# Kernel tuning notes

Measured on AMD Instinct MI355X. Metric: run time of the kernel, lower is better.

## Reference

```python
import jax, jax.numpy as jnp
import numpy as np

B, L, D_MODEL, H, DK, DV = 4, 2048, 1024, 16, 64, 64


def setup_inputs() -> dict:
    key = jax.random.key(0)
    ks = jax.random.split(key, 11)
    s = 1.0 / np.sqrt(D_MODEL)
    return {
        "queries": jax.random.normal(ks[0], (B, L, D_MODEL), jnp.float32),
        "keys": jax.random.normal(ks[1], (B, L, D_MODEL), jnp.float32),
        "values": jax.random.normal(ks[2], (B, L, D_MODEL), jnp.float32),
        "Wq": jax.random.normal(ks[3], (D_MODEL, H * DK), jnp.float32) * s,
        "bq": jnp.zeros((H * DK,), jnp.float32),
        "Wk": jax.random.normal(ks[4], (D_MODEL, H * DK), jnp.float32) * s,
        "bk": jnp.zeros((H * DK,), jnp.float32),
        "Wv": jax.random.normal(ks[5], (D_MODEL, H * DV), jnp.float32) * s,
        "bv": jnp.zeros((H * DV,), jnp.float32),
        "Wo": jax.random.normal(ks[6], (H * DV, D_MODEL), jnp.float32) * s,
        "bo": jnp.zeros((D_MODEL,), jnp.float32),
    }


def reference(queries, keys, values, Wq, bq, Wk, bk, Wv, bv, Wo, bo):
    b, l, _ = queries.shape
    s = keys.shape[1]
    q = (queries @ Wq + bq).reshape(b, l, H, DK)
    k = (keys @ Wk + bk).reshape(b, s, H, DK)
    v = (values @ Wv + bv).reshape(b, s, H, DV)
    scale = 1.0 / np.sqrt(DK)
    scores = jnp.einsum("blhe,bshe->bhls", q, k)  # [B,H,L,S]
    causal = jnp.triu(jnp.ones((l, s), bool), k=1)
    scores = jnp.where(causal[None, None], -jnp.inf, scores)
    A = jax.nn.softmax(scale * scores, axis=-1)
    out = jnp.einsum("bhls,bshd->blhd", A, v).reshape(b, l, H * DV)
    return out @ Wo + bo
```

## Files before the change

kernel.cpp:

```cpp
#include <hip/hip_runtime.h>

typedef __attribute__((ext_vector_type(8))) short s8v;
typedef __attribute__((ext_vector_type(4))) short s4v;
typedef __attribute__((ext_vector_type(4))) float f4v;
typedef __attribute__((ext_vector_type(4))) unsigned int u4v;

#define LOG2E 1.44269504088896340736f

__device__ __forceinline__ unsigned short f2bf(float f) {
    unsigned int x = __float_as_uint(f);
    return (unsigned short)((x + 0x7fffu + ((x >> 16) & 1u)) >> 16);
}
__device__ __forceinline__ s8v ld8(const unsigned short* p) {
    return *(const s8v*)p;
}

#define GLOAD_LDS(g, l) __builtin_amdgcn_global_load_lds(              \
    (const __attribute__((address_space(1))) void*)(const void*)(g),   \
    (__attribute__((address_space(3))) void*)(void*)(l), 16, 0, 0)

__global__ __launch_bounds__(256) void transpose_w4(
    const float* __restrict__ W0, const float* __restrict__ W1,
    const float* __restrict__ W2, const float* __restrict__ W3,
    unsigned short* __restrict__ T0, unsigned short* __restrict__ T1,
    unsigned short* __restrict__ T2, unsigned short* __restrict__ T3)
{
    __shared__ float tile[32][33];
    int z = blockIdx.z;
    const float* W = z == 0 ? W0 : z == 1 ? W1 : z == 2 ? W2 : W3;
    unsigned short* Wt = z == 0 ? T0 : z == 1 ? T1 : z == 2 ? T2 : T3;
    int tx = threadIdx.x, ty = threadIdx.y;
    int x = blockIdx.x * 32 + tx;
#pragma unroll
    for (int i = 0; i < 4; i++) {
        int y = blockIdx.y * 32 + ty + i * 8;
        tile[ty + i * 8][tx] = W[y * 1024 + x];
    }
    __syncthreads();
    int x2 = blockIdx.y * 32 + tx;
#pragma unroll
    for (int i = 0; i < 4; i++) {
        int y2 = blockIdx.x * 32 + ty + i * 8;
        Wt[y2 * 1024 + x2] = f2bf(tile[tx][ty + i * 8]);
    }
}

__global__ __launch_bounds__(256) void qkv_gemm(
    const float* __restrict__ Aq, const float* __restrict__ Ak,
    const float* __restrict__ Avv,
    const unsigned short* __restrict__ BtQ, const unsigned short* __restrict__ BtK,
    const unsigned short* __restrict__ BtV,
    const float* __restrict__ bq, const float* __restrict__ bk,
    const float* __restrict__ bv,
    unsigned short* __restrict__ qo, unsigned short* __restrict__ ko,
    unsigned short* __restrict__ vo, float sscale)
{
    __shared__ __align__(16) unsigned short ldsA[2][128 * 32];
    __shared__ __align__(16) unsigned short ldsB[2][128 * 32];

    int i = blockIdx.x;
    int c = i & 7, j = i >> 3;
    int bx = j & 7, zy = c * 24 + (j >> 3);
    int z = zy >> 6, by = zy & 63;

    const float* A = z == 0 ? Aq : z == 1 ? Ak : Avv;
    const unsigned short* Bt = z == 0 ? BtQ : z == 1 ? BtK : BtV;
    const float* bias = z == 0 ? bq : z == 1 ? bk : bv;
    unsigned short* out = z == 0 ? qo : z == 1 ? ko : vo;
    float oscale = z == 0 ? sscale : 1.0f;

    int tid = threadIdx.x;
    int w = tid >> 6, lane = tid & 63;
    int quad = lane >> 4, l15 = lane & 15;
    int wr = w >> 1, wc = w & 1;
    int m0 = by * 128, n0 = bx * 128;

    int arow = tid >> 1, ahs = tid & 1;
    int crow = tid >> 2, ck = (tid & 3) * 8;

    const float* ap = A + (size_t)(m0 + arow) * 1024 + ahs * 16;
    const unsigned short* bp = Bt + (size_t)(n0 + crow) * 1024 + ck;
    unsigned short* aw0 = &ldsA[0][arow * 32 + ahs * 16];
    unsigned short* aw1 = &ldsA[1][arow * 32 + ahs * 16];

    f4v acc[4][4];
#pragma unroll
    for (int m = 0; m < 4; m++)
#pragma unroll
        for (int n = 0; n < 4; n++) { f4v zz = {0.f, 0.f, 0.f, 0.f}; acc[m][n] = zz; }

    auto stageB = [&](int buf, int k0) {
        GLOAD_LDS(bp + k0, &ldsB[buf][w * 512]);
        GLOAD_LDS(bp + k0 + (size_t)64 * 1024, &ldsB[buf][2048 + w * 512]);
    };
    auto cvtwrA = [&](unsigned short* dst, f4v a0, f4v a1, f4v a2, f4v a3) {
        unsigned int w0, w1, w2, w3, w4, w5, w6, w7;
        asm("v_cvt_pk_bf16_f32 %0, %1, %2" : "=v"(w0) : "v"(a0[0]), "v"(a0[1]));
        asm("v_cvt_pk_bf16_f32 %0, %1, %2" : "=v"(w1) : "v"(a0[2]), "v"(a0[3]));
        asm("v_cvt_pk_bf16_f32 %0, %1, %2" : "=v"(w2) : "v"(a1[0]), "v"(a1[1]));
        asm("v_cvt_pk_bf16_f32 %0, %1, %2" : "=v"(w3) : "v"(a1[2]), "v"(a1[3]));
        asm("v_cvt_pk_bf16_f32 %0, %1, %2" : "=v"(w4) : "v"(a2[0]), "v"(a2[1]));
        asm("v_cvt_pk_bf16_f32 %0, %1, %2" : "=v"(w5) : "v"(a2[2]), "v"(a2[3]));
        asm("v_cvt_pk_bf16_f32 %0, %1, %2" : "=v"(w6) : "v"(a3[0]), "v"(a3[1]));
        asm("v_cvt_pk_bf16_f32 %0, %1, %2" : "=v"(w7) : "v"(a3[2]), "v"(a3[3]));
        u4v lo; lo[0] = w0; lo[1] = w1; lo[2] = w2; lo[3] = w3;
        u4v hi; hi[0] = w4; hi[1] = w5; hi[2] = w6; hi[3] = w7;
        *(u4v*)dst = lo;
        *(u4v*)(dst + 8) = hi;
    };

    {
        f4v a0 = *(const f4v*)(ap), a1 = *(const f4v*)(ap + 4);
        f4v a2 = *(const f4v*)(ap + 8), a3 = *(const f4v*)(ap + 12);
        stageB(0, 0);
        cvtwrA(aw0, a0, a1, a2, a3);
    }
    __syncthreads();

    for (int t = 0; t < 32; t++) {
        int buf = t & 1;
        bool pf = t < 31;
        f4v a0, a1, a2, a3;
        if (pf) {
            const float* an = ap + (t + 1) * 32;
            a0 = *(const f4v*)(an); a1 = *(const f4v*)(an + 4);
            a2 = *(const f4v*)(an + 8); a3 = *(const f4v*)(an + 12);
            stageB(buf ^ 1, (t + 1) * 32);
        }
        s8v af[4], bfr[4];
#pragma unroll
        for (int m = 0; m < 4; m++)
            af[m] = *(const s8v*)&ldsA[buf][(wr * 64 + m * 16 + l15) * 32 + quad * 8];
#pragma unroll
        for (int n = 0; n < 4; n++)
            bfr[n] = *(const s8v*)&ldsB[buf][(wc * 64 + n * 16 + l15) * 32 + quad * 8];
#pragma unroll
        for (int m = 0; m < 4; m++)
#pragma unroll
            for (int n = 0; n < 4; n++)
                acc[m][n] = __builtin_amdgcn_mfma_f32_16x16x32_bf16(af[m], bfr[n], acc[m][n], 0, 0, 0);
        if (pf) cvtwrA(buf ? aw0 : aw1, a0, a1, a2, a3);
        __syncthreads();
    }

#pragma unroll
    for (int n = 0; n < 4; n++) {
        int col = n0 + wc * 64 + n * 16 + l15;
        float bvf = bias[col];
#pragma unroll
        for (int m = 0; m < 4; m++) {
#pragma unroll
            for (int r = 0; r < 4; r++) {
                int row = m0 + wr * 64 + m * 16 + quad * 4 + r;
                float v = (acc[m][n][r] + bvf) * oscale;
                int bb = row >> 11, l = row & 2047;
                int hh = col >> 6, d = col & 63;
                if (z != 2) {
                    out[(((size_t)bb * 16 + hh) * 2048 + l) * 64 + d] = f2bf(v);
                } else {
                    int jj = l & 63;
                    int s = ((jj & 0x0C) << 2) | ((jj & 0x02) << 2) |
                            ((jj & 0x30) >> 3) | (jj & 1);
                    int lp = (l & ~63) | s;
                    out[(((size_t)bb * 16 + hh) * 64 + d) * 2048 + lp] = f2bf(v);
                }
            }
        }
    }
}

__global__ __launch_bounds__(256) void ogemm(
    const unsigned short* __restrict__ A,
    const unsigned short* __restrict__ Bt,
    const float* __restrict__ bias,
    float* __restrict__ out)
{
    __shared__ __align__(16) unsigned short ldsA[2][128 * 32];
    __shared__ __align__(16) unsigned short ldsB[2][128 * 32];

    int i = blockIdx.x;
    int c = i & 7, j = i >> 3;
    int bx = j & 7, by = c * 8 + (j >> 3);

    int tid = threadIdx.x;
    int w = tid >> 6, lane = tid & 63;
    int quad = lane >> 4, l15 = lane & 15;
    int wr = w >> 1, wc = w & 1;
    int m0 = by * 128, n0 = bx * 128;

    int crow = tid >> 2, ck = (tid & 3) * 8;

    f4v acc[4][4];
#pragma unroll
    for (int m = 0; m < 4; m++)
#pragma unroll
        for (int n = 0; n < 4; n++) { f4v zz = {0.f, 0.f, 0.f, 0.f}; acc[m][n] = zz; }

    auto stage = [&](int buf, int k0) {
        const unsigned short* ga = A + (size_t)(m0 + crow) * 1024 + k0 + ck;
        GLOAD_LDS(ga, &ldsA[buf][w * 512]);
        GLOAD_LDS(ga + (size_t)64 * 1024, &ldsA[buf][2048 + w * 512]);
        const unsigned short* gb = Bt + (size_t)(n0 + crow) * 1024 + k0 + ck;
        GLOAD_LDS(gb, &ldsB[buf][w * 512]);
        GLOAD_LDS(gb + (size_t)64 * 1024, &ldsB[buf][2048 + w * 512]);
    };

    stage(0, 0);
    __syncthreads();
    for (int t = 0; t < 32; t++) {
        int buf = t & 1;
        if (t < 31) stage(buf ^ 1, (t + 1) * 32);
        s8v af[4], bfr[4];
#pragma unroll
        for (int m = 0; m < 4; m++)
            af[m] = *(const s8v*)&ldsA[buf][(wr * 64 + m * 16 + l15) * 32 + quad * 8];
#pragma unroll
        for (int n = 0; n < 4; n++)
            bfr[n] = *(const s8v*)&ldsB[buf][(wc * 64 + n * 16 + l15) * 32 + quad * 8];
#pragma unroll
        for (int m = 0; m < 4; m++)
#pragma unroll
            for (int n = 0; n < 4; n++)
                acc[m][n] = __builtin_amdgcn_mfma_f32_16x16x32_bf16(af[m], bfr[n], acc[m][n], 0, 0, 0);
        __syncthreads();
    }

#pragma unroll
    for (int n = 0; n < 4; n++) {
        int col = n0 + wc * 64 + n * 16 + l15;
        float bvf = bias[col];
#pragma unroll
        for (int m = 0; m < 4; m++)
#pragma unroll
            for (int r = 0; r < 4; r++) {
                int row = m0 + wr * 64 + m * 16 + quad * 4 + r;
                out[(size_t)row * 1024 + col] = acc[m][n][r] + bvf;
            }
    }
}

__global__ __launch_bounds__(256) void attn_kernel(
    const unsigned short* __restrict__ Q,
    const unsigned short* __restrict__ K,
    const unsigned short* __restrict__ Vt,
    unsigned short* __restrict__ O)
{
    __shared__ __align__(16) unsigned short Kb[2][64 * 64];
    __shared__ __align__(16) unsigned short Vb[2][64 * 64];

    int tid = threadIdx.x;
    int w = tid >> 6, lane = tid & 63;
    int quad = lane >> 4, l15 = lane & 15;

    int bid = blockIdx.x;
    int swz = (bid & 7) * 128 + (bid >> 3);
    int xp = swz & 15;
    int h = (swz >> 4) & 15;
    int b = swz >> 8;
    int bh = b * 16 + h;

    int srow = tid >> 3;
    int soff = ((tid & 7) * 16) ^ ((srow & 7) << 4);
    const unsigned short* Kbase = K + (size_t)bh * 2048 * 64;
    const unsigned short* Vbase = Vt + (size_t)bh * 64 * 2048;

    auto stageK = [&](int buf, int kt) {
        const unsigned short* g1 = Kbase + (size_t)(kt * 64 + srow) * 64 + (soff >> 1);
        GLOAD_LDS(g1, &Kb[buf][w * 512]);
        GLOAD_LDS(g1 + (size_t)32 * 64, &Kb[buf][2048 + w * 512]);
    };
    auto stageV = [&](int buf, int kt) {
        const unsigned short* g1 = Vbase + (size_t)srow * 2048 + kt * 64 + (soff >> 1);
        GLOAD_LDS(g1, &Vb[buf][w * 512]);
        GLOAD_LDS(g1 + (size_t)32 * 2048, &Vb[buf][2048 + w * 512]);
    };

    int rswz = (l15 & 7) << 4;

#pragma unroll 1
    for (int half = 0; half < 2; half++) {
        int qt = half ? 31 - xp : xp;
        int m0 = qt * 64 + w * 16;

        const unsigned short* qb = Q + ((size_t)bh * 2048 + m0 + l15) * 64 + quad * 8;
        s8v aq0 = ld8(qb), aq1 = ld8(qb + 32);

        float mrun = -1e30f, lsum = 0.f;
        f4v oacc[4];
#pragma unroll
        for (int t = 0; t < 4; t++) { f4v z = {0.f, 0.f, 0.f, 0.f}; oacc[t] = z; }

        stageK(0, 0);
        stageV(0, 0);
        __syncthreads();

#pragma unroll 1
        for (int kt = 0; kt <= qt; kt++) {
            int buf = kt & 1;
            if (kt < qt) { stageK(buf ^ 1, kt + 1); stageV(buf ^ 1, kt + 1); }

            f4v sacc[4];
#pragma unroll
            for (int t = 0; t < 4; t++) { f4v z = {0.f, 0.f, 0.f, 0.f}; sacc[t] = z; }
            const char* kbp = (const char*)&Kb[buf][0];
#pragma unroll
            for (int t = 0; t < 4; t++) {
                int rb = (t * 16 + l15) * 128;
                s8v k0 = *(const s8v*)(kbp + rb + ((quad * 16) ^ rswz));
                s8v k1 = *(const s8v*)(kbp + rb + ((64 + quad * 16) ^ rswz));
                sacc[t] = __builtin_amdgcn_mfma_f32_16x16x32_bf16(k0, aq0, sacc[t], 0, 0, 0);
                sacc[t] = __builtin_amdgcn_mfma_f32_16x16x32_bf16(k1, aq1, sacc[t], 0, 0, 0);
            }

            if (kt == qt) {
                int qrow = w * 16 + l15;
#pragma unroll
                for (int t = 0; t < 4; t++)
#pragma unroll
                    for (int r = 0; r < 4; r++) {
                        int key = t * 16 + quad * 4 + r;
                        if (key > qrow) sacc[t][r] = -1e30f;
                    }
            }

            float mx = sacc[0][0];
#pragma unroll
            for (int t = 0; t < 4; t++)
#pragma unroll
                for (int r = 0; r < 4; r++)
                    mx = fmaxf(mx, sacc[t][r]);
            mx = fmaxf(mx, __shfl_xor(mx, 16));
            mx = fmaxf(mx, __shfl_xor(mx, 32));

            if (__any(mx > mrun + 8.0f)) {
                float mnew = fmaxf(mrun, mx);
                float alpha = exp2f(mrun - mnew);
                lsum *= alpha;
#pragma unroll
                for (int r = 0; r < 4; r++) {
                    float ar = __shfl(alpha, quad * 4 + r);
#pragma unroll
                    for (int t2 = 0; t2 < 4; t2++) oacc[t2][r] *= ar;
                }
                mrun = mnew;
            }

            float rs = 0.f;
#pragma unroll
            for (int t = 0; t < 4; t++)
#pragma unroll
                for (int r = 0; r < 4; r++) {
                    float p = exp2f(sacc[t][r] - mrun);
                    rs += p;
                    sacc[t][r] = p;
                }
            lsum += rs;

            unsigned int pwv[4][2];
#pragma unroll
            for (int t = 0; t < 4; t++) {
                asm("v_cvt_pk_bf16_f32 %0, %1, %2"
                    : "=v"(pwv[t][0]) : "v"(sacc[t][0]), "v"(sacc[t][1]));
                asm("v_cvt_pk_bf16_f32 %0, %1, %2"
                    : "=v"(pwv[t][1]) : "v"(sacc[t][2]), "v"(sacc[t][3]));
            }

            const char* vbp = (const char*)&Vb[buf][0];
#pragma unroll
            for (int c = 0; c < 2; c++) {
                u4v aw;
                aw[0] = pwv[0][c]; aw[1] = pwv[1][c];
                aw[2] = pwv[2][c]; aw[3] = pwv[3][c];
                s8v apf = __builtin_bit_cast(s8v, aw);
#pragma unroll
                for (int t2 = 0; t2 < 4; t2++) {
                    int rb = (t2 * 16 + l15) * 128;
                    s8v bvv = *(const s8v*)(vbp + rb + ((quad * 32 + c * 16) ^ rswz));
                    oacc[t2] = __builtin_amdgcn_mfma_f32_16x16x32_bf16(apf, bvv, oacc[t2], 0, 0, 0);
                }
            }
            __syncthreads();
        }

        float ltot = lsum;
        ltot += __shfl_xor(ltot, 16);
        ltot += __shfl_xor(ltot, 32);
        float inv = 1.f / ltot;
#pragma unroll
        for (int r = 0; r < 4; r++) {
            float ir = __shfl(inv, quad * 4 + r);
            int l = m0 + quad * 4 + r;
#pragma unroll
            for (int t2 = 0; t2 < 4; t2++) {
                O[((size_t)b * 2048 + l) * 1024 + h * 64 + t2 * 16 + l15] = f2bf(oacc[t2][r] * ir);
            }
        }
    }
}

extern "C" void kernel_launch(void* const* d_in, const int* in_sizes, int n_in,
                              void* d_out, int out_size, void* d_ws, size_t ws_size,
                              hipStream_t stream)
{
    const float* queries = (const float*)d_in[0];
    const float* keys    = (const float*)d_in[1];
    const float* values  = (const float*)d_in[2];
    const float* Wq = (const float*)d_in[3];
    const float* bq = (const float*)d_in[4];
    const float* Wk = (const float*)d_in[5];
    const float* bk = (const float*)d_in[6];
    const float* Wv = (const float*)d_in[7];
    const float* bv = (const float*)d_in[8];
    const float* Wo = (const float*)d_in[9];
    const float* bo = (const float*)d_in[10];

    unsigned short* ws = (unsigned short*)d_ws;
    const size_t M1 = 1u << 20, M8 = 8u << 20;
    unsigned short* WqT = ws;
    unsigned short* WkT = ws + 1 * M1;
    unsigned short* WvT = ws + 2 * M1;
    unsigned short* WoT = ws + 3 * M1;
    unsigned short* qw  = ws + 4 * M1;
    unsigned short* kw  = qw + M8;
    unsigned short* vtw = kw + M8;
    unsigned short* ow  = vtw + M8;

    const float sscale = 0.125f * LOG2E;

    dim3 tb(32, 8);
    transpose_w4<<<dim3(32, 32, 4), tb, 0, stream>>>(
        Wq, Wk, Wv, Wo, WqT, WkT, WvT, WoT);

    qkv_gemm<<<dim3(1536), 256, 0, stream>>>(
        queries, keys, values, WqT, WkT, WvT, bq, bk, bv,
        qw, kw, vtw, sscale);

    attn_kernel<<<dim3(1024), 256, 0, stream>>>(qw, kw, vtw, ow);

    ogemm<<<dim3(512), 256, 0, stream>>>(ow, WoT, bo, (float*)d_out);
}
```

Baseline: 391.7 us.

## Enlarge QKV GEMM tiles to 256x256 with 512 threads and swizzled A LDS

Grows the fused QKV projection GEMM block tile from 128x128 to 256x256, running 8 waves per block with a 128x64 sub-tile per wave. The grid shrinks from 1536 to 384 blocks with a new block-to-tile mapping. The larger tile is meant to cut global and LDS traffic per MFMA through more operand reuse. A new XOR swizzle on the A tile in LDS is meant to avoid bank conflicts on the fragment reads. In exchange it raises register pressure and LDS use, and 384 blocks spread unevenly over the CUs, which can leave a tail of idle units.

```diff
diff --git a/kernel.cpp b/kernel.cpp
--- a/kernel.cpp
+++ b/kernel.cpp
@@ -45,7 +45,7 @@
     }
 }
 
-__global__ __launch_bounds__(256) void qkv_gemm(
+__global__ __launch_bounds__(512) void qkv_gemm(
     const float* __restrict__ Aq, const float* __restrict__ Ak,
     const float* __restrict__ Avv,
     const unsigned short* __restrict__ BtQ, const unsigned short* __restrict__ BtK,
@@ -55,45 +55,48 @@
     unsigned short* __restrict__ qo, unsigned short* __restrict__ ko,
     unsigned short* __restrict__ vo, float sscale)
 {
-    __shared__ __align__(16) unsigned short ldsA[2][128 * 32];
-    __shared__ __align__(16) unsigned short ldsB[2][128 * 32];
+    __shared__ __align__(16) unsigned short ldsA[2][256 * 32];
+    __shared__ __align__(16) unsigned short ldsB[2][256 * 32];
 
     int i = blockIdx.x;
     int c = i & 7, j = i >> 3;
-    int bx = j & 7, zy = c * 24 + (j >> 3);
-    int z = zy >> 6, by = zy & 63;
-
+    int by = c * 4 + (j & 3);
+    int bx = j >> 2;
+
+    int z = bx >> 2;
     const float* A = z == 0 ? Aq : z == 1 ? Ak : Avv;
     const unsigned short* Bt = z == 0 ? BtQ : z == 1 ? BtK : BtV;
     const float* bias = z == 0 ? bq : z == 1 ? bk : bv;
     unsigned short* out = z == 0 ? qo : z == 1 ? ko : vo;
     float oscale = z == 0 ? sscale : 1.0f;
 
+    int m0 = by * 256;
+    int n0 = (bx & 3) * 256;
+
     int tid = threadIdx.x;
     int w = tid >> 6, lane = tid & 63;
     int quad = lane >> 4, l15 = lane & 15;
-    int wr = w >> 1, wc = w & 1;
-    int m0 = by * 128, n0 = bx * 128;
-
-    int arow = tid >> 1, ahs = tid & 1;
-    int crow = tid >> 2, ck = (tid & 3) * 8;
-
-    const float* ap = A + (size_t)(m0 + arow) * 1024 + ahs * 16;
-    const unsigned short* bp = Bt + (size_t)(n0 + crow) * 1024 + ck;
-    unsigned short* aw0 = &ldsA[0][arow * 32 + ahs * 16];
-    unsigned short* aw1 = &ldsA[1][arow * 32 + ahs * 16];
-
-    f4v acc[4][4];
-#pragma unroll
-    for (int m = 0; m < 4; m++)
+    int wr = w >> 2, wc = w & 3;
+
+    int arow = tid >> 1, ahalf = tid & 1;
+    const float* ap = A + (size_t)(m0 + arow) * 1024 + ahalf * 16;
+    int ab = arow * 64 + ahalf * 32;
+    int aswz = (arow & 7) << 4;
+    int awb0 = ab ^ aswz, awb1 = (ab + 16) ^ aswz;
+
+    const unsigned short* bp = Bt + (size_t)(n0 + (tid >> 2)) * 1024 + (tid & 3) * 8;
+
+    f4v acc[8][4];
+#pragma unroll
+    for (int m = 0; m < 8; m++)
 #pragma unroll
         for (int n = 0; n < 4; n++) { f4v zz = {0.f, 0.f, 0.f, 0.f}; acc[m][n] = zz; }
 
     auto stageB = [&](int buf, int k0) {
         GLOAD_LDS(bp + k0, &ldsB[buf][w * 512]);
-        GLOAD_LDS(bp + k0 + (size_t)64 * 1024, &ldsB[buf][2048 + w * 512]);
+        GLOAD_LDS(bp + k0 + (size_t)128 * 1024, &ldsB[buf][4096 + w * 512]);
     };
-    auto cvtwrA = [&](unsigned short* dst, f4v a0, f4v a1, f4v a2, f4v a3) {
+    auto cvtwrA = [&](int buf, f4v a0, f4v a1, f4v a2, f4v a3) {
         unsigned int w0, w1, w2, w3, w4, w5, w6, w7;
         asm("v_cvt_pk_bf16_f32 %0, %1, %2" : "=v"(w0) : "v"(a0[0]), "v"(a0[1]));
         asm("v_cvt_pk_bf16_f32 %0, %1, %2" : "=v"(w1) : "v"(a0[2]), "v"(a0[3]));
@@ -105,15 +108,18 @@
         asm("v_cvt_pk_bf16_f32 %0, %1, %2" : "=v"(w7) : "v"(a3[2]), "v"(a3[3]));
         u4v lo; lo[0] = w0; lo[1] = w1; lo[2] = w2; lo[3] = w3;
         u4v hi; hi[0] = w4; hi[1] = w5; hi[2] = w6; hi[3] = w7;
-        *(u4v*)dst = lo;
-        *(u4v*)(dst + 8) = hi;
+        char* base = (char*)&ldsA[buf][0];
+        *(u4v*)(base + awb0) = lo;
+        *(u4v*)(base + awb1) = hi;
     };
 
+    int rswzA = (l15 & 7) << 4;
+
     {
-        f4v a0 = *(const f4v*)(ap), a1 = *(const f4v*)(ap + 4);
+        f4v a0 = *(const f4v*)ap, a1 = *(const f4v*)(ap + 4);
         f4v a2 = *(const f4v*)(ap + 8), a3 = *(const f4v*)(ap + 12);
         stageB(0, 0);
-        cvtwrA(aw0, a0, a1, a2, a3);
+        cvtwrA(0, a0, a1, a2, a3);
     }
     __syncthreads();
 
@@ -123,23 +129,26 @@
         f4v a0, a1, a2, a3;
         if (pf) {
             const float* an = ap + (t + 1) * 32;
-            a0 = *(const f4v*)(an); a1 = *(const f4v*)(an + 4);
+            a0 = *(const f4v*)an; a1 = *(const f4v*)(an + 4);
             a2 = *(const f4v*)(an + 8); a3 = *(const f4v*)(an + 12);
             stageB(buf ^ 1, (t + 1) * 32);
         }
-        s8v af[4], bfr[4];
-#pragma unroll
-        for (int m = 0; m < 4; m++)
-            af[m] = *(const s8v*)&ldsA[buf][(wr * 64 + m * 16 + l15) * 32 + quad * 8];
+        const char* abase = (const char*)&ldsA[buf][0];
+        s8v af[8], bfr[4];
+#pragma unroll
+        for (int m = 0; m < 8; m++) {
+            int row = wr * 128 + m * 16 + l15;
+            af[m] = *(const s8v*)(abase + ((row * 64 + quad * 16) ^ rswzA));
+        }
 #pragma unroll
         for (int n = 0; n < 4; n++)
             bfr[n] = *(const s8v*)&ldsB[buf][(wc * 64 + n * 16 + l15) * 32 + quad * 8];
 #pragma unroll
-        for (int m = 0; m < 4; m++)
+        for (int m = 0; m < 8; m++)
 #pragma unroll
             for (int n = 0; n < 4; n++)
                 acc[m][n] = __builtin_amdgcn_mfma_f32_16x16x32_bf16(af[m], bfr[n], acc[m][n], 0, 0, 0);
-        if (pf) cvtwrA(buf ? aw0 : aw1, a0, a1, a2, a3);
+        if (pf) cvtwrA(buf ^ 1, a0, a1, a2, a3);
         __syncthreads();
     }
 
@@ -147,14 +156,14 @@
     for (int n = 0; n < 4; n++) {
         int col = n0 + wc * 64 + n * 16 + l15;
         float bvf = bias[col];
-#pragma unroll
-        for (int m = 0; m < 4; m++) {
+        int hh = col >> 6, d = col & 63;
+#pragma unroll
+        for (int m = 0; m < 8; m++) {
 #pragma unroll
             for (int r = 0; r < 4; r++) {
-                int row = m0 + wr * 64 + m * 16 + quad * 4 + r;
+                int row = m0 + wr * 128 + m * 16 + quad * 4 + r;
                 float v = (acc[m][n][r] + bvf) * oscale;
                 int bb = row >> 11, l = row & 2047;
-                int hh = col >> 6, d = col & 63;
                 if (z != 2) {
                     out[(((size_t)bb * 16 + hh) * 2048 + l) * 64 + d] = f2bf(v);
                 } else {
@@ -431,7 +440,7 @@
     transpose_w4<<<dim3(32, 32, 4), tb, 0, stream>>>(
         Wq, Wk, Wv, Wo, WqT, WkT, WvT, WoT);
 
-    qkv_gemm<<<dim3(1536), 256, 0, stream>>>(
+    qkv_gemm<<<dim3(384), 512, 0, stream>>>(
         queries, keys, values, WqT, WkT, WvT, bq, bk, bv,
         qw, kw, vtw, sscale);
 
```

Result: slower. 405.5 us (+3.5%).

## Triple-buffer GEMM LDS stages with swizzled layout and explicit waitcnt barriers

Applied to the files above, without the earlier changes.

Both the QKV projection GEMM and the output GEMM move from double to triple LDS buffering, prefetching two K-steps ahead. The single __syncthreads per step becomes explicit vmcnt/lgkmcnt waits plus s_barrier, and the MFMA block is wrapped in s_setprio. The LDS tiles get an XOR swizzle on 16-byte chunks to cut bank conflicts, and the QKV block-to-tile mapping is reordered so that z selects contiguous block ranges. The attention softmax max and sum become tree reductions to shorten dependency chains. In exchange, LDS use goes up, which may lower occupancy, and the hand-tuned wait counts are easy to get wrong.

```diff
diff --git a/kernel.cpp b/kernel.cpp
--- a/kernel.cpp
+++ b/kernel.cpp
@@ -45,7 +45,7 @@
     }
 }
 
-__global__ __launch_bounds__(256) void qkv_gemm(
+__global__ __launch_bounds__(256) void qkv_fused(
     const float* __restrict__ Aq, const float* __restrict__ Ak,
     const float* __restrict__ Avv,
     const unsigned short* __restrict__ BtQ, const unsigned short* __restrict__ BtK,
@@ -55,13 +55,14 @@
     unsigned short* __restrict__ qo, unsigned short* __restrict__ ko,
     unsigned short* __restrict__ vo, float sscale)
 {
-    __shared__ __align__(16) unsigned short ldsA[2][128 * 32];
-    __shared__ __align__(16) unsigned short ldsB[2][128 * 32];
+    __shared__ __align__(16) unsigned short ldsA[3][128 * 32];
+    __shared__ __align__(16) unsigned short ldsB[3][128 * 32];
 
     int i = blockIdx.x;
-    int c = i & 7, j = i >> 3;
-    int bx = j & 7, zy = c * 24 + (j >> 3);
-    int z = zy >> 6, by = zy & 63;
+    int z = i >> 9;
+    int r = i & 511;
+    int c = r & 7, j = r >> 3;
+    int bx = j & 7, by = c * 8 + (j >> 3);
 
     const float* A = z == 0 ? Aq : z == 1 ? Ak : Avv;
     const unsigned short* Bt = z == 0 ? BtQ : z == 1 ? BtK : BtV;
@@ -75,13 +76,15 @@
     int wr = w >> 1, wc = w & 1;
     int m0 = by * 128, n0 = bx * 128;
 
-    int arow = tid >> 1, ahs = tid & 1;
-    int crow = tid >> 2, ck = (tid & 3) * 8;
-
-    const float* ap = A + (size_t)(m0 + arow) * 1024 + ahs * 16;
-    const unsigned short* bp = Bt + (size_t)(n0 + crow) * 1024 + ck;
-    unsigned short* aw0 = &ldsA[0][arow * 32 + ahs * 16];
-    unsigned short* aw1 = &ldsA[1][arow * 32 + ahs * 16];
+    int r1 = tid >> 2, qp = tid & 3;
+    int qs = (qp ^ (r1 & 3)) * 8;
+    const unsigned short* gb1 = Bt + (size_t)(n0 + r1) * 1024 + qs;
+    const unsigned short* gb2 = Bt + (size_t)(n0 + r1 + 64) * 1024 + qs;
+
+    int arow = tid >> 1, ahalf = tid & 1;
+    const float* ap = A + (size_t)(m0 + arow) * 1024 + ahalf * 16;
+    int awb0 = arow * 64 + (((2 * ahalf)     ^ (arow & 3)) << 4);
+    int awb1 = arow * 64 + (((2 * ahalf + 1) ^ (arow & 3)) << 4);
 
     f4v acc[4][4];
 #pragma unroll
@@ -90,10 +93,10 @@
         for (int n = 0; n < 4; n++) { f4v zz = {0.f, 0.f, 0.f, 0.f}; acc[m][n] = zz; }
 
     auto stageB = [&](int buf, int k0) {
-        GLOAD_LDS(bp + k0, &ldsB[buf][w * 512]);
-        GLOAD_LDS(bp + k0 + (size_t)64 * 1024, &ldsB[buf][2048 + w * 512]);
+        GLOAD_LDS(gb1 + k0, &ldsB[buf][w * 512]);
+        GLOAD_LDS(gb2 + k0, &ldsB[buf][2048 + w * 512]);
     };
-    auto cvtwrA = [&](unsigned short* dst, f4v a0, f4v a1, f4v a2, f4v a3) {
+    auto cvtwrA = [&](int buf, f4v a0, f4v a1, f4v a2, f4v a3) {
         unsigned int w0, w1, w2, w3, w4, w5, w6, w7;
         asm("v_cvt_pk_bf16_f32 %0, %1, %2" : "=v"(w0) : "v"(a0[0]), "v"(a0[1]));
         asm("v_cvt_pk_bf16_f32 %0, %1, %2" : "=v"(w1) : "v"(a0[2]), "v"(a0[3]));
@@ -105,78 +108,98 @@
         asm("v_cvt_pk_bf16_f32 %0, %1, %2" : "=v"(w7) : "v"(a3[2]), "v"(a3[3]));
         u4v lo; lo[0] = w0; lo[1] = w1; lo[2] = w2; lo[3] = w3;
         u4v hi; hi[0] = w4; hi[1] = w5; hi[2] = w6; hi[3] = w7;
-        *(u4v*)dst = lo;
-        *(u4v*)(dst + 8) = hi;
+        char* base = (char*)&ldsA[buf][0];
+        *(u4v*)(base + awb0) = lo;
+        *(u4v*)(base + awb1) = hi;
     };
 
+    int xr = (l15 & 3) << 4;
+
     {
-        f4v a0 = *(const f4v*)(ap), a1 = *(const f4v*)(ap + 4);
+        f4v a0 = *(const f4v*)ap,       a1 = *(const f4v*)(ap + 4);
         f4v a2 = *(const f4v*)(ap + 8), a3 = *(const f4v*)(ap + 12);
         stageB(0, 0);
-        cvtwrA(aw0, a0, a1, a2, a3);
-    }
-    __syncthreads();
-
+        stageB(1, 32);
+        asm volatile("s_waitcnt vmcnt(2)" ::: "memory");
+        cvtwrA(0, a0, a1, a2, a3);
+        asm volatile("s_waitcnt lgkmcnt(0)" ::: "memory");
+        asm volatile("s_barrier" ::: "memory");
+    }
+
+    int buf = 0;
     for (int t = 0; t < 32; t++) {
-        int buf = t & 1;
-        bool pf = t < 31;
+        if (t < 30) {
+            int nb = buf + 2; if (nb >= 3) nb -= 3;
+            stageB(nb, (t + 2) * 32);
+        }
         f4v a0, a1, a2, a3;
-        if (pf) {
+        if (t < 31) {
             const float* an = ap + (t + 1) * 32;
-            a0 = *(const f4v*)(an); a1 = *(const f4v*)(an + 4);
+            a0 = *(const f4v*)an;       a1 = *(const f4v*)(an + 4);
             a2 = *(const f4v*)(an + 8); a3 = *(const f4v*)(an + 12);
-            stageB(buf ^ 1, (t + 1) * 32);
-        }
+        }
+        const char* ab = (const char*)&ldsA[buf][0];
+        const char* bb = (const char*)&ldsB[buf][0];
         s8v af[4], bfr[4];
 #pragma unroll
         for (int m = 0; m < 4; m++)
-            af[m] = *(const s8v*)&ldsA[buf][(wr * 64 + m * 16 + l15) * 32 + quad * 8];
+            af[m] = *(const s8v*)(ab + (wr * 64 + m * 16 + l15) * 64 + ((quad * 16) ^ xr));
 #pragma unroll
         for (int n = 0; n < 4; n++)
-            bfr[n] = *(const s8v*)&ldsB[buf][(wc * 64 + n * 16 + l15) * 32 + quad * 8];
+            bfr[n] = *(const s8v*)(bb + (wc * 64 + n * 16 + l15) * 64 + ((quad * 16) ^ xr));
+        __builtin_amdgcn_s_setprio(1);
 #pragma unroll
         for (int m = 0; m < 4; m++)
 #pragma unroll
             for (int n = 0; n < 4; n++)
                 acc[m][n] = __builtin_amdgcn_mfma_f32_16x16x32_bf16(af[m], bfr[n], acc[m][n], 0, 0, 0);
-        if (pf) cvtwrA(buf ? aw0 : aw1, a0, a1, a2, a3);
-        __syncthreads();
+        __builtin_amdgcn_s_setprio(0);
+        if (t < 31) {
+            if (t < 30) asm volatile("s_waitcnt vmcnt(2)" ::: "memory");
+            else        asm volatile("s_waitcnt vmcnt(0)" ::: "memory");
+            int nb1 = buf + 1; if (nb1 >= 3) nb1 -= 3;
+            cvtwrA(nb1, a0, a1, a2, a3);
+            asm volatile("s_waitcnt lgkmcnt(0)" ::: "memory");
+            asm volatile("s_barrier" ::: "memory");
+            __builtin_amdgcn_sched_barrier(0);
+        }
+        buf++; if (buf >= 3) buf = 0;
     }
 
 #pragma unroll
     for (int n = 0; n < 4; n++) {
         int col = n0 + wc * 64 + n * 16 + l15;
         float bvf = bias[col];
+        int hh = col >> 6, d = col & 63;
 #pragma unroll
         for (int m = 0; m < 4; m++) {
 #pragma unroll
-            for (int r = 0; r < 4; r++) {
-                int row = m0 + wr * 64 + m * 16 + quad * 4 + r;
-                float v = (acc[m][n][r] + bvf) * oscale;
-                int bb = row >> 11, l = row & 2047;
-                int hh = col >> 6, d = col & 63;
+            for (int r2 = 0; r2 < 4; r2++) {
+                int row = m0 + wr * 64 + m * 16 + quad * 4 + r2;
+                float v = (acc[m][n][r2] + bvf) * oscale;
+                int bb2 = row >> 11, l = row & 2047;
                 if (z != 2) {
-                    out[(((size_t)bb * 16 + hh) * 2048 + l) * 64 + d] = f2bf(v);
+                    out[(((size_t)bb2 * 16 + hh) * 2048 + l) * 64 + d] = f2bf(v);
                 } else {
                     int jj = l & 63;
                     int s = ((jj & 0x0C) << 2) | ((jj & 0x02) << 2) |
                             ((jj & 0x30) >> 3) | (jj & 1);
                     int lp = (l & ~63) | s;
-                    out[(((size_t)bb * 16 + hh) * 64 + d) * 2048 + lp] = f2bf(v);
+                    out[(((size_t)bb2 * 16 + hh) * 64 + d) * 2048 + lp] = f2bf(v);
                 }
             }
         }
     }
 }
 
-__global__ __launch_bounds__(256) void ogemm(
+__global__ __launch_bounds__(256) void gemm_ctd(
     const unsigned short* __restrict__ A,
     const unsigned short* __restrict__ Bt,
     const float* __restrict__ bias,
     float* __restrict__ out)
 {
-    __shared__ __align__(16) unsigned short ldsA[2][128 * 32];
-    __shared__ __align__(16) unsigned short ldsB[2][128 * 32];
+    __shared__ __align__(16) unsigned short ldsA[3][128 * 32];
+    __shared__ __align__(16) unsigned short ldsB[3][128 * 32];
 
     int i = blockIdx.x;
     int c = i & 7, j = i >> 3;
@@ -188,7 +211,12 @@
     int wr = w >> 1, wc = w & 1;
     int m0 = by * 128, n0 = bx * 128;
 
-    int crow = tid >> 2, ck = (tid & 3) * 8;
+    int r1 = tid >> 2, qp = tid & 3;
+    int qs = (qp ^ (r1 & 3)) * 8;
+    const unsigned short* ga1 = A  + (size_t)(m0 + r1) * 1024 + qs;
+    const unsigned short* ga2 = A  + (size_t)(m0 + r1 + 64) * 1024 + qs;
+    const unsigned short* gb1 = Bt + (size_t)(n0 + r1) * 1024 + qs;
+    const unsigned short* gb2 = Bt + (size_t)(n0 + r1 + 64) * 1024 + qs;
 
     f4v acc[4][4];
 #pragma unroll
@@ -197,32 +225,48 @@
         for (int n = 0; n < 4; n++) { f4v zz = {0.f, 0.f, 0.f, 0.f}; acc[m][n] = zz; }
 
     auto stage = [&](int buf, int k0) {
-        const unsigned short* ga = A + (size_t)(m0 + crow) * 1024 + k0 + ck;
-        GLOAD_LDS(ga, &ldsA[buf][w * 512]);
-        GLOAD_LDS(ga + (size_t)64 * 1024, &ldsA[buf][2048 + w * 512]);
-        const unsigned short* gb = Bt + (size_t)(n0 + crow) * 1024 + k0 + ck;
-        GLOAD_LDS(gb, &ldsB[buf][w * 512]);
-        GLOAD_LDS(gb + (size_t)64 * 1024, &ldsB[buf][2048 + w * 512]);
+        GLOAD_LDS(ga1 + k0, &ldsA[buf][w * 512]);
+        GLOAD_LDS(ga2 + k0, &ldsA[buf][2048 + w * 512]);
+        GLOAD_LDS(gb1 + k0, &ldsB[buf][w * 512]);
+        GLOAD_LDS(gb2 + k0, &ldsB[buf][2048 + w * 512]);
     };
 
+    int xr = (l15 & 3) << 4;
+
     stage(0, 0);
-    __syncthreads();
+    stage(1, 32);
+    asm volatile("s_waitcnt vmcnt(4)" ::: "memory");
+    asm volatile("s_barrier" ::: "memory");
+
+    int buf = 0;
     for (int t = 0; t < 32; t++) {
-        int buf = t & 1;
-        if (t < 31) stage(buf ^ 1, (t + 1) * 32);
+        if (t < 30) {
+            int nb = buf + 2; if (nb >= 3) nb -= 3;
+            stage(nb, (t + 2) * 32);
+        }
+        const char* ab = (const char*)&ldsA[buf][0];
+        const char* bb = (const char*)&ldsB[buf][0];
         s8v af[4], bfr[4];
 #pragma unroll
         for (int m = 0; m < 4; m++)
-            af[m] = *(const s8v*)&ldsA[buf][(wr * 64 + m * 16 + l15) * 32 + quad * 8];
+            af[m] = *(const s8v*)(ab + (wr * 64 + m * 16 + l15) * 64 + ((quad * 16) ^ xr));
 #pragma unroll
         for (int n = 0; n < 4; n++)
-            bfr[n] = *(const s8v*)&ldsB[buf][(wc * 64 + n * 16 + l15) * 32 + quad * 8];
+            bfr[n] = *(const s8v*)(bb + (wc * 64 + n * 16 + l15) * 64 + ((quad * 16) ^ xr));
+        __builtin_amdgcn_s_setprio(1);
 #pragma unroll
         for (int m = 0; m < 4; m++)
 #pragma unroll
             for (int n = 0; n < 4; n++)
                 acc[m][n] = __builtin_amdgcn_mfma_f32_16x16x32_bf16(af[m], bfr[n], acc[m][n], 0, 0, 0);
-        __syncthreads();
+        __builtin_amdgcn_s_setprio(0);
+        if (t < 31) {
+            if (t < 30) asm volatile("s_waitcnt vmcnt(4)" ::: "memory");
+            else        asm volatile("s_waitcnt vmcnt(0)" ::: "memory");
+            asm volatile("s_barrier" ::: "memory");
+            __builtin_amdgcn_sched_barrier(0);
+        }
+        buf++; if (buf >= 3) buf = 0;
     }
 
 #pragma unroll
@@ -232,9 +276,9 @@
 #pragma unroll
         for (int m = 0; m < 4; m++)
 #pragma unroll
-            for (int r = 0; r < 4; r++) {
-                int row = m0 + wr * 64 + m * 16 + quad * 4 + r;
-                out[(size_t)row * 1024 + col] = acc[m][n][r] + bvf;
+            for (int r2 = 0; r2 < 4; r2++) {
+                int row = m0 + wr * 64 + m * 16 + quad * 4 + r2;
+                out[(size_t)row * 1024 + col] = acc[m][n][r2] + bvf;
             }
     }
 }
@@ -323,12 +367,12 @@
                     }
             }
 
-            float mx = sacc[0][0];
+            float tmax[4];
 #pragma unroll
             for (int t = 0; t < 4; t++)
-#pragma unroll
-                for (int r = 0; r < 4; r++)
-                    mx = fmaxf(mx, sacc[t][r]);
+                tmax[t] = fmaxf(fmaxf(sacc[t][0], sacc[t][1]),
+                                fmaxf(sacc[t][2], sacc[t][3]));
+            float mx = fmaxf(fmaxf(tmax[0], tmax[1]), fmaxf(tmax[2], tmax[3]));
             mx = fmaxf(mx, __shfl_xor(mx, 16));
             mx = fmaxf(mx, __shfl_xor(mx, 32));
 
@@ -345,16 +389,18 @@
                 mrun = mnew;
             }
 
-            float rs = 0.f;
-#pragma unroll
-            for (int t = 0; t < 4; t++)
-#pragma unroll
-                for (int r = 0; r < 4; r++) {
-                    float p = exp2f(sacc[t][r] - mrun);
-                    rs += p;
-                    sacc[t][r] = p;
-                }
-            lsum += rs;
+            float ps[4];
+#pragma unroll
+            for (int t = 0; t < 4; t++) {
+                float p0 = exp2f(sacc[t][0] - mrun);
+                float p1 = exp2f(sacc[t][1] - mrun);
+                float p2 = exp2f(sacc[t][2] - mrun);
+                float p3 = exp2f(sacc[t][3] - mrun);
+                sacc[t][0] = p0; sacc[t][1] = p1;
+                sacc[t][2] = p2; sacc[t][3] = p3;
+                ps[t] = (p0 + p1) + (p2 + p3);
+            }
+            lsum += (ps[0] + ps[1]) + (ps[2] + ps[3]);
 
             unsigned int pwv[4][2];
 #pragma unroll
@@ -367,15 +413,15 @@
 
             const char* vbp = (const char*)&Vb[buf][0];
 #pragma unroll
-            for (int c = 0; c < 2; c++) {
+            for (int cc = 0; cc < 2; cc++) {
                 u4v aw;
-                aw[0] = pwv[0][c]; aw[1] = pwv[1][c];
-                aw[2] = pwv[2][c]; aw[3] = pwv[3][c];
+                aw[0] = pwv[0][cc]; aw[1] = pwv[1][cc];
+                aw[2] = pwv[2][cc]; aw[3] = pwv[3][cc];
                 s8v apf = __builtin_bit_cast(s8v, aw);
 #pragma unroll
                 for (int t2 = 0; t2 < 4; t2++) {
                     int rb = (t2 * 16 + l15) * 128;
-                    s8v bvv = *(const s8v*)(vbp + rb + ((quad * 32 + c * 16) ^ rswz));
+                    s8v bvv = *(const s8v*)(vbp + rb + ((quad * 32 + cc * 16) ^ rswz));
                     oacc[t2] = __builtin_amdgcn_mfma_f32_16x16x32_bf16(apf, bvv, oacc[t2], 0, 0, 0);
                 }
             }
@@ -431,11 +477,11 @@
     transpose_w4<<<dim3(32, 32, 4), tb, 0, stream>>>(
         Wq, Wk, Wv, Wo, WqT, WkT, WvT, WoT);
 
-    qkv_gemm<<<dim3(1536), 256, 0, stream>>>(
+    qkv_fused<<<dim3(1536), 256, 0, stream>>>(
         queries, keys, values, WqT, WkT, WvT, bq, bk, bv,
         qw, kw, vtw, sscale);
 
     attn_kernel<<<dim3(1024), 256, 0, stream>>>(qw, kw, vtw, ow);
 
-    ogemm<<<dim3(512), 256, 0, stream>>>(ow, WoT, bo, (float*)d_out);
-}
+    gemm_ctd<<<dim3(512), 256, 0, stream>>>(ow, WoT, bo, (float*)d_out);
+}
```

New measurement: 387.0 us. Within noise of the previous version (-1.2%).
